# Kernel optimization log

Measured on AMD Instinct MI355X. Metric: run time of the kernel, lower is better.

Reference implementation:

```python
import jax, jax.numpy as jnp
import numpy as np

B, T, E, H = 4, 2048, 1024, 16
HD = E // H  # 64


def setup_inputs() -> dict:
    key = jax.random.key(0)
    ks = jax.random.split(key, 7)
    s = 0.02
    return {
        "values": jax.random.normal(ks[0], (B, T, E), jnp.float32),
        "keys": jax.random.normal(ks[1], (B, T, E), jnp.float32),
        "query": jax.random.normal(ks[2], (B, T, E), jnp.float32),
        "Wv": jax.random.normal(ks[3], (HD, HD), jnp.float32) * s,
        "Wk": jax.random.normal(ks[4], (HD, HD), jnp.float32) * s,
        "Wq": jax.random.normal(ks[5], (HD, HD), jnp.float32) * s,
        "Wo": jax.random.normal(ks[6], (E, E), jnp.float32) * s,
    }


def _proj_split(x, W):
    # x: [B,T,E] -> per-head projection with shared [HD,HD] weight -> [B,H,T,HD]
    xh = x.reshape(B, T, H, HD)
    return jnp.einsum("bthd,ed->bhte", xh, W)  # torch Linear: x @ W.T


def reference(values, keys, query, Wv, Wk, Wq, Wo):
    v = _proj_split(values, Wv)   # [B,H,T,HD]
    k = _proj_split(keys, Wk)
    q = _proj_split(query, Wq)
    scale = 1.0 / np.sqrt(HD).astype(np.float32)
    scores = jnp.einsum("bhqd,bhkd->bhqk", q, k) * scale  # [B,H,T,T]
    probs = jax.nn.softmax(scores, axis=-1)
    attn = jnp.einsum("bhqk,bhkd->bhqd", probs, v)        # [B,H,T,HD]
    out = attn.transpose(0, 2, 1, 3).reshape(B, T, E)      # combine heads
    return out @ Wo.T
```

## Files before the change

kernel.cpp:

```cpp
#include <hip/hip_runtime.h>


typedef __bf16 bf16x8 __attribute__((ext_vector_type(8)));
typedef float f32x4 __attribute__((ext_vector_type(4)));
typedef float f32x16 __attribute__((ext_vector_type(16)));
typedef unsigned int u32x2v __attribute__((ext_vector_type(2)));
typedef unsigned int u32x4v __attribute__((ext_vector_type(4)));

#define DEVI static __device__ __forceinline__

constexpr int Bc = 4, Tc = 2048, Ec = 1024, HDc = 64;
constexpr int BHc = 64;

DEVI unsigned short f2bf(float f) {
  unsigned int u = __builtin_bit_cast(unsigned int, f);
  u += 0x7fffu + ((u >> 16) & 1u);
  return (unsigned short)(u >> 16);
}

DEVI int swzf(int row) { return (row & 7) ^ ((row >> 3) & 3); }

DEVI bf16x8 lds_frag(const unsigned short* base, int row, int chunk) {
  const char* p = reinterpret_cast<const char*>(base) + row * 128 + ((chunk ^ swzf(row)) * 16);
  return *reinterpret_cast<const bf16x8*>(p);
}
DEVI void lds_store16(unsigned short* base, int row, int ci, uint4 v) {
  char* p = reinterpret_cast<char*>(base) + row * 128 + ((ci ^ swzf(row)) * 16);
  *reinterpret_cast<uint4*>(p) = v;
}
DEVI uint4 pack8(float4 a, float4 b) {
  uint4 o;
  o.x = f2bf(a.x) | ((unsigned)f2bf(a.y) << 16);
  o.y = f2bf(a.z) | ((unsigned)f2bf(a.w) << 16);
  o.z = f2bf(b.x) | ((unsigned)f2bf(b.y) << 16);
  o.w = f2bf(b.z) | ((unsigned)f2bf(b.w) << 16);
  return o;
}

DEVI unsigned cvt_pk_bf16(float lo, float hi) {
  unsigned r;
  asm("v_cvt_pk_bf16_f32 %0, %1, %2" : "=v"(r) : "v"(lo), "v"(hi));
  return r;
}
DEVI float exp2_fast(float x) {
  float r;
  asm("v_exp_f32 %0, %1" : "=v"(r) : "v"(x));
  return r;
}
DEVI void plswap(unsigned& a, unsigned& b) {
#if __has_builtin(__builtin_amdgcn_permlane32_swap)
  u32x2v r = __builtin_amdgcn_permlane32_swap(a, b, false, false);
  a = r.x; b = r.y;
#else
  int lane = threadIdx.x & 63;
  unsigned sa = (unsigned)__shfl_xor((int)a, 32), sb = (unsigned)__shfl_xor((int)b, 32);
  unsigned na = (lane < 32) ? a : sb;
  unsigned nb = (lane < 32) ? sa : b;
  a = na; b = nb;
#endif
}
DEVI float halfsum(float x) {
  unsigned a = __builtin_bit_cast(unsigned, x), b = a;
  plswap(a, b);
  return __builtin_bit_cast(float, a) + __builtin_bit_cast(float, b);
}

DEVI void gload16(const unsigned short* g, unsigned short* l) {
  __builtin_amdgcn_global_load_lds(
      (const __attribute__((address_space(1))) void*)g,
      (__attribute__((address_space(3))) void*)l, 16, 0, 0);
}

__global__ __launch_bounds__(256) void proj3_kernel(
    const float* __restrict__ xv, const float* __restrict__ xk,
    const float* __restrict__ xq, const float* __restrict__ Wv,
    const float* __restrict__ Wk, const float* __restrict__ Wq,
    unsigned short* __restrict__ ov, unsigned short* __restrict__ ok,
    unsigned short* __restrict__ oq, float qscale) {
  const int which = blockIdx.z;
  const float* x = which == 0 ? xv : which == 1 ? xk : xq;
  const float* W = which == 0 ? Wv : which == 1 ? Wk : Wq;
  unsigned short* out = which == 0 ? ov : which == 1 ? ok : oq;
  const int transposed = (which == 0);
  const float wscale = (which == 2) ? qscale : 1.0f;

  __shared__ __align__(16) unsigned short Xl[64 * 64];
  __shared__ __align__(16) unsigned short Wl[64 * 64];
  const int tid = threadIdx.x;
  const int bh = blockIdx.y, t0 = blockIdx.x * 64;
  const int b = bh >> 4, h = bh & 15;
  const float* xbase = x + (size_t)(b * Tc + t0) * Ec + h * HDc;

#pragma unroll
  for (int it = 0; it < 2; ++it) {
    int ch = tid + it * 256;
    int row = ch >> 3, ci = ch & 7;
    float4 wa = *reinterpret_cast<const float4*>(W + row * 64 + ci * 8);
    float4 wb = *reinterpret_cast<const float4*>(W + row * 64 + ci * 8 + 4);
    wa.x *= wscale; wa.y *= wscale; wa.z *= wscale; wa.w *= wscale;
    wb.x *= wscale; wb.y *= wscale; wb.z *= wscale; wb.w *= wscale;
    lds_store16(Wl, row, ci, pack8(wa, wb));
    float4 xa = *reinterpret_cast<const float4*>(xbase + (size_t)row * Ec + ci * 8);
    float4 xb = *reinterpret_cast<const float4*>(xbase + (size_t)row * Ec + ci * 8 + 4);
    lds_store16(Xl, row, ci, pack8(xa, xb));
  }
  __syncthreads();

  const int lane = tid & 63, wv = tid >> 6;
  const int c16 = lane & 15, hi = lane >> 4;
  f32x4 acc[4];
#pragma unroll
  for (int nb = 0; nb < 4; ++nb) acc[nb] = {0.f, 0.f, 0.f, 0.f};
  if (!transposed) {
#pragma unroll
    for (int c = 0; c < 2; ++c) {
      bf16x8 aX = lds_frag(Xl, 16 * wv + c16, 4 * c + hi);
#pragma unroll
      for (int nb = 0; nb < 4; ++nb) {
        bf16x8 bW = lds_frag(Wl, 16 * nb + c16, 4 * c + hi);
        acc[nb] = __builtin_amdgcn_mfma_f32_16x16x32_bf16(aX, bW, acc[nb], 0, 0, 0);
      }
    }
#pragma unroll
    for (int nb = 0; nb < 4; ++nb)
#pragma unroll
      for (int r = 0; r < 4; ++r) {
        int t = t0 + 16 * wv + 4 * hi + r;
        int e = 16 * nb + c16;
        out[(size_t)(bh * Tc + t) * HDc + e] = f2bf(acc[nb][r]);
      }
  } else {
#pragma unroll
    for (int c = 0; c < 2; ++c) {
      bf16x8 aW = lds_frag(Wl, 16 * wv + c16, 4 * c + hi);
#pragma unroll
      for (int nb = 0; nb < 4; ++nb) {
        bf16x8 bX = lds_frag(Xl, 16 * nb + c16, 4 * c + hi);
        acc[nb] = __builtin_amdgcn_mfma_f32_16x16x32_bf16(aW, bX, acc[nb], 0, 0, 0);
      }
    }
#pragma unroll
    for (int nb = 0; nb < 4; ++nb)
#pragma unroll
      for (int r = 0; r < 4; ++r) {
        int e = 16 * wv + 4 * hi + r;
        int t = t0 + 16 * nb + c16;
        out[(size_t)(bh * HDc + e) * Tc + t] = f2bf(acc[nb][r]);
      }
  }
}

__global__ __launch_bounds__(256) void cast_wo(const float* __restrict__ Wsrc,
                                               unsigned short* __restrict__ dst) {
  size_t i = (size_t)blockIdx.x * 256 + threadIdx.x;
  float4 f = *reinterpret_cast<const float4*>(Wsrc + i * 4);
  uint2 o;
  o.x = f2bf(f.x) | ((unsigned)f2bf(f.y) << 16);
  o.y = f2bf(f.z) | ((unsigned)f2bf(f.w) << 16);
  *reinterpret_cast<uint2*>(dst + i * 4) = o;
}

DEVI void stage_kv(const unsigned short* __restrict__ Kp,
                   const unsigned short* __restrict__ Vp, int kt,
                   unsigned short* Kl, unsigned short* Vl, int wv, int lane) {
#pragma unroll
  for (int j = 0; j < 2; ++j) {
    const int base = (4 * j + wv) * 64;
    const int slot = base + lane;
    const int row = slot >> 3;
    const int sc = ((slot & 7) ^ swzf(row)) * 8;
    gload16(Kp + (size_t)(kt * 64 + row) * 64 + sc, Kl + base * 8);
    gload16(Vp + (size_t)row * Tc + kt * 64 + sc, Vl + base * 8);
  }
}

DEVI float exp_sum_pf(f32x16& s0, f32x16& s1, bf16x8 pf[4]) {
#pragma unroll
  for (int i = 0; i < 16; ++i) s0[i] = exp2_fast(s0[i]);
#pragma unroll
  for (int i = 0; i < 16; ++i) s1[i] = exp2_fast(s1[i]);
  float t[16];
#pragma unroll
  for (int i = 0; i < 16; ++i) t[i] = s0[i] + s1[i];
#pragma unroll
  for (int i = 0; i < 8; ++i) t[i] += t[i + 8];
#pragma unroll
  for (int i = 0; i < 4; ++i) t[i] += t[i + 4];
  float rs = (t[0] + t[1]) + (t[2] + t[3]);
  unsigned w0[8], w1[8];
#pragma unroll
  for (int i = 0; i < 8; ++i) w0[i] = cvt_pk_bf16(s0[2 * i], s0[2 * i + 1]);
#pragma unroll
  for (int i = 0; i < 8; ++i) w1[i] = cvt_pk_bf16(s1[2 * i], s1[2 * i + 1]);
  plswap(w0[0], w0[2]); plswap(w0[1], w0[3]); plswap(w0[4], w0[6]); plswap(w0[5], w0[7]);
  plswap(w1[0], w1[2]); plswap(w1[1], w1[3]); plswap(w1[4], w1[6]); plswap(w1[5], w1[7]);
  pf[0] = __builtin_bit_cast(bf16x8, (u32x4v){w0[0], w0[1], w0[2], w0[3]});
  pf[1] = __builtin_bit_cast(bf16x8, (u32x4v){w0[4], w0[5], w0[6], w0[7]});
  pf[2] = __builtin_bit_cast(bf16x8, (u32x4v){w1[0], w1[1], w1[2], w1[3]});
  pf[3] = __builtin_bit_cast(bf16x8, (u32x4v){w1[4], w1[5], w1[6], w1[7]});
  return rs;
}

__global__ __launch_bounds__(256, 2) void attn_kernel(
    const unsigned short* __restrict__ Qb_, const unsigned short* __restrict__ Kb_,
    const unsigned short* __restrict__ Vtb_, unsigned short* __restrict__ O) {
  __shared__ __align__(16) unsigned short KV[4][2][64 * 64];
  const int tid = threadIdx.x, lane = tid & 63, wv = tid >> 6;
  const int c32 = lane & 31, hi = lane >> 5;
  const int flat = blockIdx.y * (int)gridDim.x + blockIdx.x;
  const int logical = (flat & 7) * 64 + (flat >> 3);
  const int q0 = (logical & 7) * 256, bh = logical >> 3;
  const int b = bh >> 4, h = bh & 15;
  const unsigned short* Qp = Qb_ + (size_t)bh * Tc * HDc;
  const unsigned short* Kp = Kb_ + (size_t)bh * Tc * HDc;
  const unsigned short* Vp = Vtb_ + (size_t)bh * HDc * Tc;

  const int tA = q0 + 64 * wv + c32, tB = tA + 32;
  bf16x8 qfA[4], qfB[4];
#pragma unroll
  for (int c = 0; c < 4; ++c) {
    qfA[c] = *reinterpret_cast<const bf16x8*>(Qp + (size_t)tA * HDc + 16 * c + 8 * hi);
    qfB[c] = *reinterpret_cast<const bf16x8*>(Qp + (size_t)tB * HDc + 16 * c + 8 * hi);
  }

  stage_kv(Kp, Vp, 0, KV[0][0], KV[0][1], wv, lane);
  stage_kv(Kp, Vp, 1, KV[1][0], KV[1][1], wv, lane);

  f32x16 aA0, aA1, aB0, aB1, zv;
#pragma unroll
  for (int i = 0; i < 16; ++i) {
    aA0[i] = 0.f; aA1[i] = 0.f; aB0[i] = 0.f; aB1[i] = 0.f; zv[i] = 0.f;
  }
  float lA = 0.f, lB = 0.f;

  auto tile = [&](const unsigned short* Kl, const unsigned short* Vl) {
    f32x16 sA0, sA1, sB0, sB1;
    __builtin_amdgcn_s_setprio(1);
    {
      bf16x8 k0 = lds_frag(Kl, c32, hi);
      sA0 = __builtin_amdgcn_mfma_f32_32x32x16_bf16(k0, qfA[0], zv, 0, 0, 0);
      sB0 = __builtin_amdgcn_mfma_f32_32x32x16_bf16(k0, qfB[0], zv, 0, 0, 0);
      bf16x8 k1 = lds_frag(Kl, 32 + c32, hi);
      sA1 = __builtin_amdgcn_mfma_f32_32x32x16_bf16(k1, qfA[0], zv, 0, 0, 0);
      sB1 = __builtin_amdgcn_mfma_f32_32x32x16_bf16(k1, qfB[0], zv, 0, 0, 0);
    }
#pragma unroll
    for (int c = 1; c < 4; ++c) {
      bf16x8 k0 = lds_frag(Kl, c32, 2 * c + hi);
      sA0 = __builtin_amdgcn_mfma_f32_32x32x16_bf16(k0, qfA[c], sA0, 0, 0, 0);
      sB0 = __builtin_amdgcn_mfma_f32_32x32x16_bf16(k0, qfB[c], sB0, 0, 0, 0);
      bf16x8 k1 = lds_frag(Kl, 32 + c32, 2 * c + hi);
      sA1 = __builtin_amdgcn_mfma_f32_32x32x16_bf16(k1, qfA[c], sA1, 0, 0, 0);
      sB1 = __builtin_amdgcn_mfma_f32_32x32x16_bf16(k1, qfB[c], sB1, 0, 0, 0);
    }
    __builtin_amdgcn_s_setprio(0);
    bf16x8 pfA[4], pfB[4];
    lA += exp_sum_pf(sA0, sA1, pfA);
    lB += exp_sum_pf(sB0, sB1, pfB);
    __builtin_amdgcn_s_setprio(1);
#pragma unroll
    for (int ks = 0; ks < 4; ++ks) {
      bf16x8 v0 = lds_frag(Vl, c32, 2 * ks + hi);
      aA0 = __builtin_amdgcn_mfma_f32_32x32x16_bf16(v0, pfA[ks], aA0, 0, 0, 0);
      aB0 = __builtin_amdgcn_mfma_f32_32x32x16_bf16(v0, pfB[ks], aB0, 0, 0, 0);
      bf16x8 v1 = lds_frag(Vl, 32 + c32, 2 * ks + hi);
      aA1 = __builtin_amdgcn_mfma_f32_32x32x16_bf16(v1, pfA[ks], aA1, 0, 0, 0);
      aB1 = __builtin_amdgcn_mfma_f32_32x32x16_bf16(v1, pfB[ks], aB1, 0, 0, 0);
    }
    __builtin_amdgcn_s_setprio(0);
  };

  constexpr int NT = Tc / 64;
  for (int t = 0; t < NT; ++t) {
    if (t + 2 < NT) {
      stage_kv(Kp, Vp, t + 2, KV[(t + 2) & 3][0], KV[(t + 2) & 3][1], wv, lane);
      asm volatile("s_waitcnt vmcnt(8)" ::: "memory");
    } else if (t + 1 < NT) {
      asm volatile("s_waitcnt vmcnt(4)" ::: "memory");
    } else {
      asm volatile("s_waitcnt vmcnt(0)" ::: "memory");
    }
    __builtin_amdgcn_s_barrier();
    tile(KV[t & 3][0], KV[t & 3][1]);
  }

  {
    const float rl = 1.0f / halfsum(lA);
    unsigned short* orow = O + (size_t)(b * Tc + tA) * Ec + h * HDc;
#pragma unroll
    for (int rq = 0; rq < 4; ++rq) {
      uint2 p0, p1;
      p0.x = cvt_pk_bf16(aA0[4 * rq] * rl, aA0[4 * rq + 1] * rl);
      p0.y = cvt_pk_bf16(aA0[4 * rq + 2] * rl, aA0[4 * rq + 3] * rl);
      *reinterpret_cast<uint2*>(orow + 8 * rq + 4 * hi) = p0;
      p1.x = cvt_pk_bf16(aA1[4 * rq] * rl, aA1[4 * rq + 1] * rl);
      p1.y = cvt_pk_bf16(aA1[4 * rq + 2] * rl, aA1[4 * rq + 3] * rl);
      *reinterpret_cast<uint2*>(orow + 32 + 8 * rq + 4 * hi) = p1;
    }
  }
  {
    const float rl = 1.0f / halfsum(lB);
    unsigned short* orow = O + (size_t)(b * Tc + tB) * Ec + h * HDc;
#pragma unroll
    for (int rq = 0; rq < 4; ++rq) {
      uint2 p0, p1;
      p0.x = cvt_pk_bf16(aB0[4 * rq] * rl, aB0[4 * rq + 1] * rl);
      p0.y = cvt_pk_bf16(aB0[4 * rq + 2] * rl, aB0[4 * rq + 3] * rl);
      *reinterpret_cast<uint2*>(orow + 8 * rq + 4 * hi) = p0;
      p1.x = cvt_pk_bf16(aB1[4 * rq] * rl, aB1[4 * rq + 1] * rl);
      p1.y = cvt_pk_bf16(aB1[4 * rq + 2] * rl, aB1[4 * rq + 3] * rl);
      *reinterpret_cast<uint2*>(orow + 32 + 8 * rq + 4 * hi) = p1;
    }
  }
}

DEVI void stage_ab(const unsigned short* __restrict__ Ap,
                   const unsigned short* __restrict__ Bp, int kt,
                   unsigned short* Al, unsigned short* Bl, int wv, int lane) {
#pragma unroll
  for (int j = 0; j < 4; ++j) {
    const int base = (4 * j + wv) * 64;
    const int slot = base + lane;
    const int row = slot >> 3;
    const int sc = ((slot & 7) ^ swzf(row)) * 8;
    gload16(Ap + (size_t)row * Ec + kt * 64 + sc, Al + base * 8);
    gload16(Bp + (size_t)row * Ec + kt * 64 + sc, Bl + base * 8);
  }
}

__global__ __launch_bounds__(256, 2) void ogemm_kernel(
    const unsigned short* __restrict__ A, const unsigned short* __restrict__ Bw,
    float* __restrict__ out) {
  __shared__ __align__(16) unsigned short Al[2][128 * 64];
  __shared__ __align__(16) unsigned short Bl[2][128 * 64];
  const int tid = threadIdx.x, lane = tid & 63, wv = tid >> 6;
  const int c32 = lane & 31, hi = lane >> 5;
  const int flat = blockIdx.y * (int)gridDim.x + blockIdx.x;
  const int logical = (flat & 7) * 64 + (flat >> 3);
  const int n0 = (logical & 7) * 128, m0 = (logical >> 3) * 128;
  const int wr = wv >> 1, wc = wv & 1;
  const unsigned short* Ap = A + (size_t)m0 * Ec;
  const unsigned short* Bp = Bw + (size_t)n0 * Ec;

  f32x16 acc[2][2];
#pragma unroll
  for (int mi = 0; mi < 2; ++mi)
#pragma unroll
    for (int ni = 0; ni < 2; ++ni)
#pragma unroll
      for (int i = 0; i < 16; ++i) acc[mi][ni][i] = 0.f;

  auto gtile = [&](const unsigned short* Alc, const unsigned short* Blc) {
    __builtin_amdgcn_s_setprio(1);
#pragma unroll
    for (int kc = 0; kc < 4; ++kc) {
      bf16x8 x0 = lds_frag(Alc, 64 * wr + c32, 2 * kc + hi);
      bf16x8 x1 = lds_frag(Alc, 64 * wr + 32 + c32, 2 * kc + hi);
      bf16x8 y0 = lds_frag(Blc, 64 * wc + c32, 2 * kc + hi);
      bf16x8 y1 = lds_frag(Blc, 64 * wc + 32 + c32, 2 * kc + hi);
      acc[0][0] = __builtin_amdgcn_mfma_f32_32x32x16_bf16(x0, y0, acc[0][0], 0, 0, 0);
      acc[0][1] = __builtin_amdgcn_mfma_f32_32x32x16_bf16(x0, y1, acc[0][1], 0, 0, 0);
      acc[1][0] = __builtin_amdgcn_mfma_f32_32x32x16_bf16(x1, y0, acc[1][0], 0, 0, 0);
      acc[1][1] = __builtin_amdgcn_mfma_f32_32x32x16_bf16(x1, y1, acc[1][1], 0, 0, 0);
    }
    __builtin_amdgcn_s_setprio(0);
  };

  stage_ab(Ap, Bp, 0, Al[0], Bl[0], wv, lane);
  __syncthreads();
  for (int kt = 0; kt < Ec / 64; kt += 2) {
    stage_ab(Ap, Bp, kt + 1, Al[1], Bl[1], wv, lane);
    gtile(Al[0], Bl[0]);
    __syncthreads();
    if (kt + 2 < Ec / 64) stage_ab(Ap, Bp, kt + 2, Al[0], Bl[0], wv, lane);
    gtile(Al[1], Bl[1]);
    __syncthreads();
  }

  const int nb = n0 + 64 * wc + c32;
  const int mb = m0 + 64 * wr + 4 * hi;
#pragma unroll
  for (int mi = 0; mi < 2; ++mi)
#pragma unroll
    for (int ni = 0; ni < 2; ++ni)
#pragma unroll
      for (int rq = 0; rq < 4; ++rq)
#pragma unroll
        for (int j = 0; j < 4; ++j) {
          int mrow = mb + 32 * mi + 8 * rq + j;
          out[(size_t)mrow * Ec + nb + 32 * ni] = acc[mi][ni][4 * rq + j];
        }
}

extern "C" void kernel_launch(void* const* d_in, const int* in_sizes, int n_in,
                              void* d_out, int out_size, void* d_ws, size_t ws_size,
                              hipStream_t stream) {
  (void)in_sizes; (void)n_in; (void)out_size; (void)ws_size;
  const float* values = (const float*)d_in[0];
  const float* keys   = (const float*)d_in[1];
  const float* query  = (const float*)d_in[2];
  const float* Wv = (const float*)d_in[3];
  const float* Wk = (const float*)d_in[4];
  const float* Wq = (const float*)d_in[5];
  const float* Wo = (const float*)d_in[6];
  float* out = (float*)d_out;

  char* ws = (char*)d_ws;
  constexpr size_t SZ = (size_t)BHc * Tc * HDc * 2;
  unsigned short* qb  = (unsigned short*)(ws + 0 * SZ);
  unsigned short* kb  = (unsigned short*)(ws + 1 * SZ);
  unsigned short* vt  = (unsigned short*)(ws + 2 * SZ);
  unsigned short* at  = (unsigned short*)(ws + 3 * SZ);
  unsigned short* wob = (unsigned short*)(ws + 4 * SZ);

  dim3 blk(256);
  proj3_kernel<<<dim3(Tc / 64, BHc, 3), blk, 0, stream>>>(
      values, keys, query, Wv, Wk, Wq, vt, kb, qb, 0.18033688011112042f);
  cast_wo<<<dim3(Ec * Ec / 1024), blk, 0, stream>>>(Wo, wob);
  attn_kernel<<<dim3(Tc / 256, BHc), blk, 0, stream>>>(qb, kb, vt, at);
  ogemm_kernel<<<dim3(Ec / 128, (Bc * Tc) / 128), blk, 0, stream>>>(at, wob, out);
}
```

Baseline: 125.8 us.

## Split attention KV sequence across two wave groups per block and reduce in LDS

The attention block grows from 256 to 512 threads. Each half of the waves processes half of the key/value sequence in 32-key tiles with its own LDS ring buffer, and the two halves' partial accumulators and row sums are then combined through LDS before normalization and store. The aim is more waves per CU and a shorter per-wave serial loop, so latency hides better. In exchange it adds an LDS reduction step with extra barriers, and the smaller tiles mean more barriers and global loads per unit of work.

```diff
diff --git a/kernel.cpp b/kernel.cpp
--- a/kernel.cpp
+++ b/kernel.cpp
@@ -160,52 +160,42 @@
   *reinterpret_cast<uint2*>(dst + i * 4) = o;
 }
 
-DEVI void stage_kv(const unsigned short* __restrict__ Kp,
-                   const unsigned short* __restrict__ Vp, int kt,
-                   unsigned short* Kl, unsigned short* Vl, int wv, int lane) {
-#pragma unroll
-  for (int j = 0; j < 2; ++j) {
-    const int base = (4 * j + wv) * 64;
-    const int slot = base + lane;
-    const int row = slot >> 3;
-    const int sc = ((slot & 7) ^ swzf(row)) * 8;
-    gload16(Kp + (size_t)(kt * 64 + row) * 64 + sc, Kl + base * 8);
-    gload16(Vp + (size_t)row * Tc + kt * 64 + sc, Vl + base * 8);
-  }
-}
-
-DEVI float exp_sum_pf(f32x16& s0, f32x16& s1, bf16x8 pf[4]) {
-#pragma unroll
-  for (int i = 0; i < 16; ++i) s0[i] = exp2_fast(s0[i]);
-#pragma unroll
-  for (int i = 0; i < 16; ++i) s1[i] = exp2_fast(s1[i]);
-  float t[16];
-#pragma unroll
-  for (int i = 0; i < 16; ++i) t[i] = s0[i] + s1[i];
-#pragma unroll
-  for (int i = 0; i < 8; ++i) t[i] += t[i + 8];
+DEVI void stage_kv32(const unsigned short* __restrict__ Kp,
+                     const unsigned short* __restrict__ Vp, int ktabs,
+                     unsigned short* Kl, unsigned short* Vl, int wl, int lane) {
+  const int row = wl * 8 + (lane >> 3);
+  const int lc = (lane & 7) ^ swzf(row);
+  gload16(Kp + (size_t)(ktabs * 32 + row) * 64 + lc * 8, Kl + wl * 512);
+  const int d = row + ((lc >> 2) << 5);
+  const int kvo = (lc & 3) * 8;
+  gload16(Vp + (size_t)d * Tc + ktabs * 32 + kvo, Vl + wl * 512);
+}
+
+DEVI float exp_sum_pf32(f32x16& s, bf16x8 pf[2]) {
+#pragma unroll
+  for (int i = 0; i < 16; ++i) s[i] = exp2_fast(s[i]);
+  float t[8];
+#pragma unroll
+  for (int i = 0; i < 8; ++i) t[i] = s[i] + s[i + 8];
 #pragma unroll
   for (int i = 0; i < 4; ++i) t[i] += t[i + 4];
   float rs = (t[0] + t[1]) + (t[2] + t[3]);
-  unsigned w0[8], w1[8];
-#pragma unroll
-  for (int i = 0; i < 8; ++i) w0[i] = cvt_pk_bf16(s0[2 * i], s0[2 * i + 1]);
-#pragma unroll
-  for (int i = 0; i < 8; ++i) w1[i] = cvt_pk_bf16(s1[2 * i], s1[2 * i + 1]);
-  plswap(w0[0], w0[2]); plswap(w0[1], w0[3]); plswap(w0[4], w0[6]); plswap(w0[5], w0[7]);
-  plswap(w1[0], w1[2]); plswap(w1[1], w1[3]); plswap(w1[4], w1[6]); plswap(w1[5], w1[7]);
-  pf[0] = __builtin_bit_cast(bf16x8, (u32x4v){w0[0], w0[1], w0[2], w0[3]});
-  pf[1] = __builtin_bit_cast(bf16x8, (u32x4v){w0[4], w0[5], w0[6], w0[7]});
-  pf[2] = __builtin_bit_cast(bf16x8, (u32x4v){w1[0], w1[1], w1[2], w1[3]});
-  pf[3] = __builtin_bit_cast(bf16x8, (u32x4v){w1[4], w1[5], w1[6], w1[7]});
+  unsigned w[8];
+#pragma unroll
+  for (int i = 0; i < 8; ++i) w[i] = cvt_pk_bf16(s[2 * i], s[2 * i + 1]);
+  plswap(w[0], w[2]); plswap(w[1], w[3]); plswap(w[4], w[6]); plswap(w[5], w[7]);
+  pf[0] = __builtin_bit_cast(bf16x8, (u32x4v){w[0], w[1], w[2], w[3]});
+  pf[1] = __builtin_bit_cast(bf16x8, (u32x4v){w[4], w[5], w[6], w[7]});
   return rs;
 }
 
-__global__ __launch_bounds__(256, 2) void attn_kernel(
+__global__ __launch_bounds__(512, 4) void attn_kernel(
     const unsigned short* __restrict__ Qb_, const unsigned short* __restrict__ Kb_,
     const unsigned short* __restrict__ Vtb_, unsigned short* __restrict__ O) {
-  __shared__ __align__(16) unsigned short KV[4][2][64 * 64];
+  __shared__ __align__(16) unsigned short KV[2][4][2][32 * 64];
+  __shared__ float lex[4][2][64];
   const int tid = threadIdx.x, lane = tid & 63, wv = tid >> 6;
+  const int wl = wv & 3, half = wv >> 2;
   const int c32 = lane & 31, hi = lane >> 5;
   const int flat = blockIdx.y * (int)gridDim.x + blockIdx.x;
   const int logical = (flat & 7) * 64 + (flat >> 3);
@@ -215,7 +205,7 @@
   const unsigned short* Kp = Kb_ + (size_t)bh * Tc * HDc;
   const unsigned short* Vp = Vtb_ + (size_t)bh * HDc * Tc;
 
-  const int tA = q0 + 64 * wv + c32, tB = tA + 32;
+  const int tA = q0 + 64 * wl + c32, tB = tA + 32;
   bf16x8 qfA[4], qfB[4];
 #pragma unroll
   for (int c = 0; c < 4; ++c) {
@@ -223,8 +213,9 @@
     qfB[c] = *reinterpret_cast<const bf16x8*>(Qp + (size_t)tB * HDc + 16 * c + 8 * hi);
   }
 
-  stage_kv(Kp, Vp, 0, KV[0][0], KV[0][1], wv, lane);
-  stage_kv(Kp, Vp, 1, KV[1][0], KV[1][1], wv, lane);
+  const int kt0 = half * 32;
+  stage_kv32(Kp, Vp, kt0 + 0, KV[half][0][0], KV[half][0][1], wl, lane);
+  stage_kv32(Kp, Vp, kt0 + 1, KV[half][1][0], KV[half][1][1], wl, lane);
 
   f32x16 aA0, aA1, aB0, aB1, zv;
 #pragma unroll
@@ -234,82 +225,107 @@
   float lA = 0.f, lB = 0.f;
 
   auto tile = [&](const unsigned short* Kl, const unsigned short* Vl) {
-    f32x16 sA0, sA1, sB0, sB1;
+    f32x16 sA, sB;
     __builtin_amdgcn_s_setprio(1);
     {
-      bf16x8 k0 = lds_frag(Kl, c32, hi);
-      sA0 = __builtin_amdgcn_mfma_f32_32x32x16_bf16(k0, qfA[0], zv, 0, 0, 0);
-      sB0 = __builtin_amdgcn_mfma_f32_32x32x16_bf16(k0, qfB[0], zv, 0, 0, 0);
-      bf16x8 k1 = lds_frag(Kl, 32 + c32, hi);
-      sA1 = __builtin_amdgcn_mfma_f32_32x32x16_bf16(k1, qfA[0], zv, 0, 0, 0);
-      sB1 = __builtin_amdgcn_mfma_f32_32x32x16_bf16(k1, qfB[0], zv, 0, 0, 0);
+      bf16x8 k = lds_frag(Kl, c32, hi);
+      sA = __builtin_amdgcn_mfma_f32_32x32x16_bf16(k, qfA[0], zv, 0, 0, 0);
+      sB = __builtin_amdgcn_mfma_f32_32x32x16_bf16(k, qfB[0], zv, 0, 0, 0);
     }
 #pragma unroll
     for (int c = 1; c < 4; ++c) {
-      bf16x8 k0 = lds_frag(Kl, c32, 2 * c + hi);
-      sA0 = __builtin_amdgcn_mfma_f32_32x32x16_bf16(k0, qfA[c], sA0, 0, 0, 0);
-      sB0 = __builtin_amdgcn_mfma_f32_32x32x16_bf16(k0, qfB[c], sB0, 0, 0, 0);
-      bf16x8 k1 = lds_frag(Kl, 32 + c32, 2 * c + hi);
-      sA1 = __builtin_amdgcn_mfma_f32_32x32x16_bf16(k1, qfA[c], sA1, 0, 0, 0);
-      sB1 = __builtin_amdgcn_mfma_f32_32x32x16_bf16(k1, qfB[c], sB1, 0, 0, 0);
+      bf16x8 k = lds_frag(Kl, c32, 2 * c + hi);
+      sA = __builtin_amdgcn_mfma_f32_32x32x16_bf16(k, qfA[c], sA, 0, 0, 0);
+      sB = __builtin_amdgcn_mfma_f32_32x32x16_bf16(k, qfB[c], sB, 0, 0, 0);
     }
     __builtin_amdgcn_s_setprio(0);
-    bf16x8 pfA[4], pfB[4];
-    lA += exp_sum_pf(sA0, sA1, pfA);
-    lB += exp_sum_pf(sB0, sB1, pfB);
+    bf16x8 pfA[2], pfB[2];
+    lA += exp_sum_pf32(sA, pfA);
+    lB += exp_sum_pf32(sB, pfB);
     __builtin_amdgcn_s_setprio(1);
 #pragma unroll
-    for (int ks = 0; ks < 4; ++ks) {
+    for (int ks = 0; ks < 2; ++ks) {
       bf16x8 v0 = lds_frag(Vl, c32, 2 * ks + hi);
       aA0 = __builtin_amdgcn_mfma_f32_32x32x16_bf16(v0, pfA[ks], aA0, 0, 0, 0);
       aB0 = __builtin_amdgcn_mfma_f32_32x32x16_bf16(v0, pfB[ks], aB0, 0, 0, 0);
-      bf16x8 v1 = lds_frag(Vl, 32 + c32, 2 * ks + hi);
+      bf16x8 v1 = lds_frag(Vl, c32, 4 + 2 * ks + hi);
       aA1 = __builtin_amdgcn_mfma_f32_32x32x16_bf16(v1, pfA[ks], aA1, 0, 0, 0);
       aB1 = __builtin_amdgcn_mfma_f32_32x32x16_bf16(v1, pfB[ks], aB1, 0, 0, 0);
     }
     __builtin_amdgcn_s_setprio(0);
   };
 
-  constexpr int NT = Tc / 64;
-  for (int t = 0; t < NT; ++t) {
-    if (t + 2 < NT) {
-      stage_kv(Kp, Vp, t + 2, KV[(t + 2) & 3][0], KV[(t + 2) & 3][1], wv, lane);
-      asm volatile("s_waitcnt vmcnt(8)" ::: "memory");
-    } else if (t + 1 < NT) {
+  constexpr int NTH = 32;
+  for (int t = 0; t < NTH; ++t) {
+    if (t + 2 < NTH) {
+      stage_kv32(Kp, Vp, kt0 + t + 2, KV[half][(t + 2) & 3][0],
+                 KV[half][(t + 2) & 3][1], wl, lane);
       asm volatile("s_waitcnt vmcnt(4)" ::: "memory");
+    } else if (t + 1 < NTH) {
+      asm volatile("s_waitcnt vmcnt(2)" ::: "memory");
     } else {
       asm volatile("s_waitcnt vmcnt(0)" ::: "memory");
     }
     __builtin_amdgcn_s_barrier();
-    tile(KV[t & 3][0], KV[t & 3][1]);
-  }
-
-  {
-    const float rl = 1.0f / halfsum(lA);
-    unsigned short* orow = O + (size_t)(b * Tc + tA) * Ec + h * HDc;
-#pragma unroll
-    for (int rq = 0; rq < 4; ++rq) {
-      uint2 p0, p1;
-      p0.x = cvt_pk_bf16(aA0[4 * rq] * rl, aA0[4 * rq + 1] * rl);
-      p0.y = cvt_pk_bf16(aA0[4 * rq + 2] * rl, aA0[4 * rq + 3] * rl);
-      *reinterpret_cast<uint2*>(orow + 8 * rq + 4 * hi) = p0;
-      p1.x = cvt_pk_bf16(aA1[4 * rq] * rl, aA1[4 * rq + 1] * rl);
-      p1.y = cvt_pk_bf16(aA1[4 * rq + 2] * rl, aA1[4 * rq + 3] * rl);
-      *reinterpret_cast<uint2*>(orow + 32 + 8 * rq + 4 * hi) = p1;
-    }
-  }
-  {
-    const float rl = 1.0f / halfsum(lB);
-    unsigned short* orow = O + (size_t)(b * Tc + tB) * Ec + h * HDc;
-#pragma unroll
-    for (int rq = 0; rq < 4; ++rq) {
-      uint2 p0, p1;
-      p0.x = cvt_pk_bf16(aB0[4 * rq] * rl, aB0[4 * rq + 1] * rl);
-      p0.y = cvt_pk_bf16(aB0[4 * rq + 2] * rl, aB0[4 * rq + 3] * rl);
-      *reinterpret_cast<uint2*>(orow + 8 * rq + 4 * hi) = p0;
-      p1.x = cvt_pk_bf16(aB1[4 * rq] * rl, aB1[4 * rq + 1] * rl);
-      p1.y = cvt_pk_bf16(aB1[4 * rq + 2] * rl, aB1[4 * rq + 3] * rl);
-      *reinterpret_cast<uint2*>(orow + 32 + 8 * rq + 4 * hi) = p1;
+    tile(KV[half][t & 3][0], KV[half][t & 3][1]);
+  }
+
+  __syncthreads();
+  float* ex = reinterpret_cast<float*>(&KV[0][0][0][0]) + wl * 4096;
+  if (half == 1) {
+#pragma unroll
+    for (int v = 0; v < 4; ++v) {
+      const f32x16& a = v == 0 ? aA0 : v == 1 ? aA1 : v == 2 ? aB0 : aB1;
+#pragma unroll
+      for (int c = 0; c < 4; ++c) {
+        f32x4 q = {a[4 * c], a[4 * c + 1], a[4 * c + 2], a[4 * c + 3]};
+        *reinterpret_cast<f32x4*>(ex + (v * 4 + c) * 256 + lane * 4) = q;
+      }
+    }
+    lex[wl][0][lane] = lA;
+    lex[wl][1][lane] = lB;
+  }
+  __syncthreads();
+  if (half == 0) {
+#pragma unroll
+    for (int v = 0; v < 4; ++v) {
+      f32x16& a = v == 0 ? aA0 : v == 1 ? aA1 : v == 2 ? aB0 : aB1;
+#pragma unroll
+      for (int c = 0; c < 4; ++c) {
+        f32x4 q = *reinterpret_cast<const f32x4*>(ex + (v * 4 + c) * 256 + lane * 4);
+        a[4 * c] += q[0]; a[4 * c + 1] += q[1]; a[4 * c + 2] += q[2]; a[4 * c + 3] += q[3];
+      }
+    }
+    lA += lex[wl][0][lane];
+    lB += lex[wl][1][lane];
+
+    {
+      const float rl = 1.0f / halfsum(lA);
+      unsigned short* orow = O + (size_t)(b * Tc + tA) * Ec + h * HDc;
+#pragma unroll
+      for (int rq = 0; rq < 4; ++rq) {
+        uint2 p0, p1;
+        p0.x = cvt_pk_bf16(aA0[4 * rq] * rl, aA0[4 * rq + 1] * rl);
+        p0.y = cvt_pk_bf16(aA0[4 * rq + 2] * rl, aA0[4 * rq + 3] * rl);
+        *reinterpret_cast<uint2*>(orow + 8 * rq + 4 * hi) = p0;
+        p1.x = cvt_pk_bf16(aA1[4 * rq] * rl, aA1[4 * rq + 1] * rl);
+        p1.y = cvt_pk_bf16(aA1[4 * rq + 2] * rl, aA1[4 * rq + 3] * rl);
+        *reinterpret_cast<uint2*>(orow + 32 + 8 * rq + 4 * hi) = p1;
+      }
+    }
+    {
+      const float rl = 1.0f / halfsum(lB);
+      unsigned short* orow = O + (size_t)(b * Tc + tB) * Ec + h * HDc;
+#pragma unroll
+      for (int rq = 0; rq < 4; ++rq) {
+        uint2 p0, p1;
+        p0.x = cvt_pk_bf16(aB0[4 * rq] * rl, aB0[4 * rq + 1] * rl);
+        p0.y = cvt_pk_bf16(aB0[4 * rq + 2] * rl, aB0[4 * rq + 3] * rl);
+        *reinterpret_cast<uint2*>(orow + 8 * rq + 4 * hi) = p0;
+        p1.x = cvt_pk_bf16(aB1[4 * rq] * rl, aB1[4 * rq + 1] * rl);
+        p1.y = cvt_pk_bf16(aB1[4 * rq + 2] * rl, aB1[4 * rq + 3] * rl);
+        *reinterpret_cast<uint2*>(orow + 32 + 8 * rq + 4 * hi) = p1;
+      }
     }
   }
 }
@@ -417,6 +433,6 @@
   proj3_kernel<<<dim3(Tc / 64, BHc, 3), blk, 0, stream>>>(
       values, keys, query, Wv, Wk, Wq, vt, kb, qb, 0.18033688011112042f);
   cast_wo<<<dim3(Ec * Ec / 1024), blk, 0, stream>>>(Wo, wob);
-  attn_kernel<<<dim3(Tc / 256, BHc), blk, 0, stream>>>(qb, kb, vt, at);
+  attn_kernel<<<dim3(Tc / 256, BHc), dim3(512), 0, stream>>>(qb, kb, vt, at);
   ogemm_kernel<<<dim3(Ec / 128, (Bc * Tc) / 128), blk, 0, stream>>>(at, wob, out);
 }
```

Result: slower. 348.1 us (+176.7%).
